# Optimization experiments

Measured on AMD Instinct MI355X. Metric: run time of the kernel, lower is better.

The kernel has to match this reference:

```python
import jax, jax.numpy as jnp
import numpy as np

N, D, DB, E, H = 1024, 512, 64, 32768, 1024

def setup_inputs() -> dict:
    key = jax.random.key(0)
    k = jax.random.split(key, 6)
    object_feats = jax.random.normal(k[0], (N, D), dtype=jnp.float32)
    bboxes_embedding = jax.random.normal(k[1], (N, N, DB), dtype=jnp.float32)
    pairs = jax.random.randint(k[2], (E, 2), 0, N, dtype=jnp.int64)
    # Kaiming-normal-ish init for the two Linear layers
    W1 = jax.random.normal(k[3], (D + D + DB, H), dtype=jnp.float32) * np.sqrt(2.0 / (D + D + DB))
    b1 = jnp.zeros((H,), dtype=jnp.float32)
    W2 = jax.random.normal(k[4], (H, D), dtype=jnp.float32) * np.sqrt(2.0 / H)
    b2 = jnp.zeros((D,), dtype=jnp.float32)
    return {"object_feats": object_feats, "bboxes_embedding": bboxes_embedding,
            "pairs": pairs, "W1": W1, "b1": b1, "W2": W2, "b2": b2}

def reference(object_feats, bboxes_embedding, pairs, W1, b1, W2, b2):
    sub = pairs[:, 0]
    obj = pairs[:, 1]
    # gather pair features: [E, D] each, plus pairwise bbox embedding [E, DB]
    f_sub = object_feats[sub]
    f_obj = object_feats[obj]
    bb = bboxes_embedding[sub, obj]
    x = jnp.concatenate((f_sub, f_obj, bb), axis=1)  # [E, 2D+DB]
    h = jax.nn.relu(x @ W1 + b1)
    out = h @ W2 + b2  # [E, D]
    n = object_feats.shape[0]
    # scatter-mean into subject nodes; each node's own feature is included once,
    # so new_feat[i] = (object_feats[i] + sum_{pairs with sub==i} out) / (1 + count[i]).
    # Nodes with no incident pairs keep their original feature (count==0 -> identity).
    seg_sum = jax.ops.segment_sum(out, sub, num_segments=n)  # [N, D]
    count = jax.ops.segment_sum(jnp.ones((out.shape[0],), dtype=out.dtype), sub, num_segments=n)
    new_feats = (object_feats + seg_sum) / (1.0 + count)[:, None]
    return (new_feats, bboxes_embedding, pairs)
```

## Files before the change

kernel.cpp:

```cpp
#include <hip/hip_runtime.h>

#define N_OBJ 1024
#define E_P   32768

typedef float f32x4 __attribute__((ext_vector_type(4)));
typedef short bf16x8 __attribute__((ext_vector_type(8)));
typedef unsigned short u16x4 __attribute__((ext_vector_type(4)));

__device__ __forceinline__ unsigned short f2bf(float f) {
    unsigned u = __float_as_uint(f);
    u = u + 0x7FFFu + ((u >> 16) & 1u);
    return (unsigned short)(u >> 16);
}

#define OFF_A    0
#define LEN_A    2097152
#define OFF_B    (OFF_A + LEN_A)
#define LEN_B    2621440
#define OFF_SEG  (OFF_B + LEN_B)
#define LEN_SEG  9437184
#define OFF_OUT  (OFF_SEG + LEN_SEG)
#define LEN_OUT  2621440

__device__ __forceinline__ void copy_role(const float4* __restrict__ src,
                                          float4* __restrict__ dst,
                                          int off, int len, int nb, int cb) {
    int stride = nb * 256;
    int i = off + cb * 256 + threadIdx.x;
    int end = off + len;
    for (; i + stride < end; i += 2 * stride) {
        float4 a = src[i];
        float4 b = src[i + stride];
        dst[i] = a;
        dst[i + stride] = b;
    }
    if (i < end) dst[i] = src[i];
}

__global__ __launch_bounds__(256) void k_a(const float* __restrict__ W1,
                                           const float* __restrict__ W2,
                                           const float* __restrict__ feats,
                                           const int* __restrict__ pairs,
                                           unsigned short* __restrict__ w1pqT,
                                           unsigned short* __restrict__ w1cT,
                                           unsigned short* __restrict__ w2T,
                                           unsigned short* __restrict__ featsb,
                                           float* __restrict__ out_pairs,
                                           int* __restrict__ counts,
                                           int* __restrict__ rank,
                                           const float4* __restrict__ csrc,
                                           float4* __restrict__ cdst) {
    int bid = blockIdx.x, tid = threadIdx.x;
    if ((bid % 3) == 2) { copy_role(csrc, cdst, OFF_A, LEN_A, 1056, bid / 3); return; }
    int job = (bid / 3) * 2 + (bid % 3);
    if (job >= 1856) {
        int i = (job - 1856) * 256 + tid;
        out_pairs[i] = (float)pairs[i];
        if (i < E_P) rank[i] = atomicAdd(&counts[pairs[2 * i]], 1);
        return;
    }
    if (job >= 1600) {
        int base = (job - 1600) * 2048 + tid * 8;
        float4 v0 = *(const float4*)&feats[base];
        float4 v1 = *(const float4*)&feats[base + 4];
        u16x4 o0 = { f2bf(v0.x), f2bf(v0.y), f2bf(v0.z), f2bf(v0.w) };
        u16x4 o1 = { f2bf(v1.x), f2bf(v1.y), f2bf(v1.z), f2bf(v1.w) };
        *(u16x4*)&featsb[base] = o0;
        *(u16x4*)&featsb[base + 4] = o1;
        return;
    }
    const float* in; unsigned short* out;
    int LDI, LDO, r0, c0, nbase, kbase;
    if (job < 1024) {
        r0 = (job >> 5) * 32; c0 = (job & 31) * 32;
        in = W1; LDI = 1024; out = w1pqT; LDO = 512;
        nbase = c0 + (r0 >= 512 ? 1024 : 0); kbase = r0 & 511;
    } else if (job < 1088) {
        int t = job - 1024; r0 = 1024 + (t >> 5) * 32; c0 = (t & 31) * 32;
        in = W1; LDI = 1024; out = w1cT; LDO = 64;
        nbase = c0; kbase = r0 - 1024;
    } else {
        int t = job - 1088; r0 = (t >> 4) * 32; c0 = (t & 15) * 32;
        in = W2; LDI = 512; out = w2T; LDO = 1024;
        nbase = c0; kbase = r0;
    }
    __shared__ float lds[32][33];
    int ti = tid >> 3, tj = (tid & 7) * 4;
    float4 v = *(const float4*)&in[(size_t)(r0 + ti) * LDI + c0 + tj];
    lds[ti][tj] = v.x; lds[ti][tj + 1] = v.y; lds[ti][tj + 2] = v.z; lds[ti][tj + 3] = v.w;
    __syncthreads();
    int oc = tid >> 3, oj = (tid & 7) * 4;
    u16x4 o = { f2bf(lds[oj][oc]), f2bf(lds[oj + 1][oc]),
                f2bf(lds[oj + 2][oc]), f2bf(lds[oj + 3][oc]) };
    *(u16x4*)&out[(size_t)(nbase + oc) * LDO + kbase + oj] = o;
}

__global__ __launch_bounds__(256) void k_b(const int* __restrict__ counts,
                                           const int* __restrict__ rank,
                                           const int* __restrict__ pairs,
                                           int* __restrict__ csr_obj,
                                           unsigned* __restrict__ brec,
                                           int* __restrict__ bcnt,
                                           const unsigned short* __restrict__ featsb,
                                           const unsigned short* __restrict__ w1pqT,
                                           const float* __restrict__ b1,
                                           float* __restrict__ P, float* __restrict__ Q,
                                           const float4* __restrict__ csrc,
                                           float4* __restrict__ cdst) {
    int bid = blockIdx.x, tid = threadIdx.x;
    if ((bid & 1) == 0) { copy_role(csrc, cdst, OFF_B, LEN_B, 672, bid >> 1); return; }
    int role = bid >> 1;
    if (role >= 641) return;

    if (role >= 129) {
        int job = role - 129;
        int m0 = (job >> 5) * 64, n0 = (job & 31) * 64;
        int w = tid >> 6, l = tid & 63;
        int ln = l & 15, kb = (l >> 4) * 8;
        int row = m0 + w * 16 + ln;
        f32x4 acc[4] = {};
        for (int k0 = 0; k0 < 512; k0 += 32) {
            bf16x8 a = *(const bf16x8*)&featsb[(size_t)row * 512 + k0 + kb];
            #pragma unroll
            for (int f = 0; f < 4; ++f) {
                bf16x8 b = *(const bf16x8*)&w1pqT[(size_t)(n0 + f * 16 + ln) * 512 + k0 + kb];
                acc[f] = __builtin_amdgcn_mfma_f32_16x16x32_bf16(a, b, acc[f], 0, 0, 0);
            }
        }
        int mr = m0 + w * 16 + (l >> 4) * 4;
        if (n0 < 1024) {
            #pragma unroll
            for (int f = 0; f < 4; ++f) {
                int n = n0 + f * 16 + ln;
                float b1v = b1[n];
                #pragma unroll
                for (int r = 0; r < 4; ++r)
                    P[(size_t)(mr + r) * 1024 + n] = acc[f][r] + b1v;
            }
        } else {
            #pragma unroll
            for (int f = 0; f < 4; ++f) {
                int n = n0 - 1024 + f * 16 + ln;
                #pragma unroll
                for (int r = 0; r < 4; ++r)
                    Q[(size_t)(mr + r) * 1024 + n] = acc[f][r];
            }
        }
        return;
    }

    __shared__ int sbuf[2][256];
    __shared__ int soff[1024];
    int c[4]; int s = 0;
    #pragma unroll
    for (int i = 0; i < 4; ++i) { c[i] = counts[tid * 4 + i]; s += c[i]; }
    sbuf[0][tid] = s;
    __syncthreads();
    int sel = 0;
    for (int d = 1; d < 256; d <<= 1) {
        int v = sbuf[sel][tid];
        if (tid >= d) v += sbuf[sel][tid - d];
        sbuf[sel ^ 1][tid] = v;
        sel ^= 1;
        __syncthreads();
    }
    int base = sbuf[sel][tid] - s;
    int run = base;
    #pragma unroll
    for (int i = 0; i < 4; ++i) { soff[tid * 4 + i] = run; run += c[i]; }
    __syncthreads();

    if (role >= 1) {
        int e = (role - 1) * 256 + tid;
        int sub = pairs[2 * e];
        csr_obj[soff[sub] + rank[e]] = pairs[2 * e + 1];
        return;
    }

    int nb[4]; int t = 0;
    #pragma unroll
    for (int i = 0; i < 4; ++i) { nb[i] = (c[i] + 31) >> 5; t += nb[i]; }
    __syncthreads();
    sbuf[0][tid] = t;
    __syncthreads();
    sel = 0;
    for (int d = 1; d < 256; d <<= 1) {
        int v = sbuf[sel][tid];
        if (tid >= d) v += sbuf[sel][tid - d];
        sbuf[sel ^ 1][tid] = v;
        sel ^= 1;
        __syncthreads();
    }
    int bpos = sbuf[sel][tid] - t;
    int run2 = base;
    #pragma unroll
    for (int i = 0; i < 4; ++i) {
        int seg = tid * 4 + i;
        for (int k = 0; k < nb[i]; ++k) {
            int st = run2 + k * 32;
            int cnt = c[i] - k * 32; if (cnt > 32) cnt = 32;
            brec[bpos++] = (unsigned)st | ((unsigned)seg << 16) | ((unsigned)(cnt - 1) << 26);
        }
        run2 += c[i];
    }
    if (tid == 255) bcnt[0] = bpos;
}

__global__ __launch_bounds__(256) void k_seg(const int* __restrict__ csr_obj,
                                             const unsigned* __restrict__ brec,
                                             const int* __restrict__ bcnt,
                                             const float* __restrict__ bb,
                                             const unsigned short* __restrict__ w1cT,
                                             const float* __restrict__ P,
                                             const float* __restrict__ Q,
                                             float* __restrict__ HS,
                                             const float4* __restrict__ csrc,
                                             float4* __restrict__ cdst) {
    int bid = blockIdx.x;
    if ((bid % 2) == 0) { copy_role(csrc, cdst, OFF_SEG, LEN_SEG, 2048, bid / 2); return; }
    int b = bid / 2;
    if (b >= bcnt[0]) return;
    unsigned rec = brec[b];
    const int start = rec & 0xFFFF;
    const int seg = (rec >> 16) & 0x3FF;
    const int n = ((rec >> 26) & 31) + 1;

    const int tid = threadIdx.x, w = tid >> 6, l = tid & 63;
    const int ln = l & 15, g4 = l >> 4, kb = g4 * 8;
    const int n0 = w * 256;
    const int nA = n < 16 ? n : 16;
    const int nB = n - 16;

    int iA = start + (ln < nA ? ln : nA - 1);
    int iB = (nB > 0) ? (start + 16 + (ln < nB ? ln : nB - 1)) : iA;
    int objA = csr_obj[iA];
    int objB = csr_obj[iB];

    const float* brA = &bb[((size_t)seg * 1024 + (size_t)objA) * 64];
    const float* brB = &bb[((size_t)seg * 1024 + (size_t)objB) * 64];
    float4 a0 = *(const float4*)&brA[kb];
    float4 a1 = *(const float4*)&brA[kb + 4];
    float4 a2 = *(const float4*)&brA[32 + kb];
    float4 a3 = *(const float4*)&brA[32 + kb + 4];
    float4 c0 = *(const float4*)&brB[kb];
    float4 c1 = *(const float4*)&brB[kb + 4];
    float4 c2 = *(const float4*)&brB[32 + kb];
    float4 c3 = *(const float4*)&brB[32 + kb + 4];
    bf16x8 A0a, A1a, A0b, A1b;
    A0a[0] = (short)f2bf(a0.x); A0a[1] = (short)f2bf(a0.y); A0a[2] = (short)f2bf(a0.z); A0a[3] = (short)f2bf(a0.w);
    A0a[4] = (short)f2bf(a1.x); A0a[5] = (short)f2bf(a1.y); A0a[6] = (short)f2bf(a1.z); A0a[7] = (short)f2bf(a1.w);
    A1a[0] = (short)f2bf(a2.x); A1a[1] = (short)f2bf(a2.y); A1a[2] = (short)f2bf(a2.z); A1a[3] = (short)f2bf(a2.w);
    A1a[4] = (short)f2bf(a3.x); A1a[5] = (short)f2bf(a3.y); A1a[6] = (short)f2bf(a3.z); A1a[7] = (short)f2bf(a3.w);
    A0b[0] = (short)f2bf(c0.x); A0b[1] = (short)f2bf(c0.y); A0b[2] = (short)f2bf(c0.z); A0b[3] = (short)f2bf(c0.w);
    A0b[4] = (short)f2bf(c1.x); A0b[5] = (short)f2bf(c1.y); A0b[6] = (short)f2bf(c1.z); A0b[7] = (short)f2bf(c1.w);
    A1b[0] = (short)f2bf(c2.x); A1b[1] = (short)f2bf(c2.y); A1b[2] = (short)f2bf(c2.z); A1b[3] = (short)f2bf(c2.w);
    A1b[4] = (short)f2bf(c3.x); A1b[5] = (short)f2bf(c3.y); A1b[6] = (short)f2bf(c3.z); A1b[7] = (short)f2bf(c3.w);

    int raA0 = __shfl(objA, g4 * 4 + 0), raA1 = __shfl(objA, g4 * 4 + 1);
    int raA2 = __shfl(objA, g4 * 4 + 2), raA3 = __shfl(objA, g4 * 4 + 3);
    int raB0 = __shfl(objB, g4 * 4 + 0), raB1 = __shfl(objB, g4 * 4 + 1);
    int raB2 = __shfl(objB, g4 * 4 + 2), raB3 = __shfl(objB, g4 * 4 + 3);
    bool vA0 = (g4 * 4 + 0) < nA, vA1 = (g4 * 4 + 1) < nA;
    bool vA2 = (g4 * 4 + 2) < nA, vA3 = (g4 * 4 + 3) < nA;
    bool vB0 = (g4 * 4 + 0) < nB, vB1 = (g4 * 4 + 1) < nB;
    bool vB2 = (g4 * 4 + 2) < nB, vB3 = (g4 * 4 + 3) < nB;

    #pragma unroll 4
    for (int f = 0; f < 16; ++f) {
        int col = n0 + f * 16 + ln;
        const unsigned short* wr = &w1cT[(size_t)col * 64];
        bf16x8 b0 = *(const bf16x8*)&wr[kb];
        bf16x8 b1 = *(const bf16x8*)&wr[32 + kb];
        f32x4 dA = {0.f, 0.f, 0.f, 0.f};
        dA = __builtin_amdgcn_mfma_f32_16x16x32_bf16(A0a, b0, dA, 0, 0, 0);
        dA = __builtin_amdgcn_mfma_f32_16x16x32_bf16(A1a, b1, dA, 0, 0, 0);
        f32x4 dB = {0.f, 0.f, 0.f, 0.f};
        dB = __builtin_amdgcn_mfma_f32_16x16x32_bf16(A0b, b0, dB, 0, 0, 0);
        dB = __builtin_amdgcn_mfma_f32_16x16x32_bf16(A1b, b1, dB, 0, 0, 0);
        float pv = P[(size_t)seg * 1024 + col];
        float qA0 = Q[(size_t)raA0 * 1024 + col];
        float qA1 = Q[(size_t)raA1 * 1024 + col];
        float qA2 = Q[(size_t)raA2 * 1024 + col];
        float qA3 = Q[(size_t)raA3 * 1024 + col];
        float qB0 = Q[(size_t)raB0 * 1024 + col];
        float qB1 = Q[(size_t)raB1 * 1024 + col];
        float qB2 = Q[(size_t)raB2 * 1024 + col];
        float qB3 = Q[(size_t)raB3 * 1024 + col];
        float h = 0.f;
        h += vA0 ? fmaxf(dA[0] + pv + qA0, 0.f) : 0.f;
        h += vA1 ? fmaxf(dA[1] + pv + qA1, 0.f) : 0.f;
        h += vA2 ? fmaxf(dA[2] + pv + qA2, 0.f) : 0.f;
        h += vA3 ? fmaxf(dA[3] + pv + qA3, 0.f) : 0.f;
        h += vB0 ? fmaxf(dB[0] + pv + qB0, 0.f) : 0.f;
        h += vB1 ? fmaxf(dB[1] + pv + qB1, 0.f) : 0.f;
        h += vB2 ? fmaxf(dB[2] + pv + qB2, 0.f) : 0.f;
        h += vB3 ? fmaxf(dB[3] + pv + qB3, 0.f) : 0.f;
        h += __shfl_xor(h, 16);
        h += __shfl_xor(h, 32);
        if (l < 16) atomicAdd(&HS[(size_t)seg * 1024 + n0 + f * 16 + l], h);
    }
}

__global__ __launch_bounds__(256) void k_out(const float* __restrict__ HS,
                                             const unsigned short* __restrict__ w2T,
                                             const float* __restrict__ feats,
                                             const float* __restrict__ b2,
                                             const int* __restrict__ counts,
                                             float* __restrict__ out0,
                                             const float4* __restrict__ csrc,
                                             float4* __restrict__ cdst) {
    int bid = blockIdx.x;
    if ((bid % 9) != 8) { copy_role(csrc, cdst, OFF_OUT, LEN_OUT, 1024, (bid / 9) * 8 + (bid % 9)); return; }
    int job = bid / 9;
    int m0 = (job >> 3) * 64, n0 = (job & 7) * 64;
    int tid = threadIdx.x, w = tid >> 6, l = tid & 63;
    int ln = l & 15, kb = (l >> 4) * 8;
    int row = m0 + w * 16 + ln;
    f32x4 acc[4] = {};
    for (int k0 = 0; k0 < 1024; k0 += 32) {
        const float* hp = &HS[(size_t)row * 1024 + k0 + kb];
        float4 h0 = *(const float4*)&hp[0];
        float4 h1 = *(const float4*)&hp[4];
        bf16x8 a;
        a[0] = (short)f2bf(h0.x); a[1] = (short)f2bf(h0.y); a[2] = (short)f2bf(h0.z); a[3] = (short)f2bf(h0.w);
        a[4] = (short)f2bf(h1.x); a[5] = (short)f2bf(h1.y); a[6] = (short)f2bf(h1.z); a[7] = (short)f2bf(h1.w);
        #pragma unroll
        for (int f = 0; f < 4; ++f) {
            bf16x8 b = *(const bf16x8*)&w2T[(size_t)(n0 + f * 16 + ln) * 1024 + k0 + kb];
            acc[f] = __builtin_amdgcn_mfma_f32_16x16x32_bf16(a, b, acc[f], 0, 0, 0);
        }
    }
    int mr = m0 + w * 16 + (l >> 4) * 4;
    float cv[4], inv[4];
    #pragma unroll
    for (int r = 0; r < 4; ++r) {
        float c = (float)counts[mr + r];
        cv[r] = c;
        inv[r] = 1.0f / (1.0f + c);
    }
    #pragma unroll
    for (int f = 0; f < 4; ++f) {
        int n = n0 + f * 16 + ln;
        float b2v = b2[n];
        #pragma unroll
        for (int r = 0; r < 4; ++r) {
            float fv = feats[(size_t)(mr + r) * 512 + n];
            out0[(size_t)(mr + r) * 512 + n] = (fv + acc[f][r] + cv[r] * b2v) * inv[r];
        }
    }
}

extern "C" void kernel_launch(void* const* d_in, const int* in_sizes, int n_in,
                              void* d_out, int out_size, void* d_ws, size_t ws_size,
                              hipStream_t stream) {
    const float* feats = (const float*)d_in[0];
    const float* bb    = (const float*)d_in[1];
    const int*   pairs = (const int*)d_in[2];
    const float* W1    = (const float*)d_in[3];
    const float* b1    = (const float*)d_in[4];
    const float* W2    = (const float*)d_in[5];
    const float* b2    = (const float*)d_in[6];

    float* out        = (float*)d_out;
    float* out_feats  = out;
    float* out_bb     = out + (size_t)N_OBJ * 512;
    float* out_pairs  = out + (size_t)N_OBJ * 512 + (size_t)N_OBJ * N_OBJ * 64;

    char* w = (char*)d_ws;
    unsigned short* featsb = (unsigned short*)w;
    unsigned short* w1pqT  = (unsigned short*)(w + (1u << 20));
    float*          HS     = (float*)w;
    unsigned short* w1cT   = (unsigned short*)(w + (4u << 20));
    unsigned short* w2T    = (unsigned short*)(w + (4u << 20) + (128u << 10));
    float* P = (float*)(w + (5u << 20) + (128u << 10));
    float* Q = (float*)(w + (9u << 20) + (128u << 10));
    char* ints = w + (13u << 20) + (128u << 10);
    int*      counts  = (int*)ints;
    int*      csr_obj = (int*)(ints + 4096);
    unsigned* brec    = (unsigned*)(ints + 4096 + 131072);
    int*      bcnt    = (int*)(ints + 4096 + 131072 + 16384);
    int*      rank    = (int*)(ints + 4096 + 131072 + 16384 + 64);

    const float4* cbb  = (const float4*)bb;
    float4*       cobb = (float4*)out_bb;

    hipMemsetAsync(counts, 0, 4096, stream);

    k_a<<<3168, 256, 0, stream>>>(W1, W2, feats, pairs, w1pqT, w1cT, w2T, featsb,
                                  out_pairs, counts, rank, cbb, cobb);
    k_b<<<1344, 256, 0, stream>>>(counts, rank, pairs, csr_obj, brec, bcnt,
                                  featsb, w1pqT, b1, P, Q, cbb, cobb);

    hipMemsetAsync(HS, 0, (size_t)N_OBJ * 1024 * sizeof(float), stream);

    k_seg<<<4096, 256, 0, stream>>>(csr_obj, brec, bcnt, bb, w1cT, P, Q, HS, cbb, cobb);
    k_out<<<1152, 256, 0, stream>>>(HS, w2T, feats, b2, counts, out_feats, cbb, cobb);
}
```

Before: 229.7 us.

## Redistribute bbox copy across kernels, drop copy from k_seg, hoist P loads

```diff
diff --git a/kernel.cpp b/kernel.cpp
--- a/kernel.cpp
+++ b/kernel.cpp
@@ -14,13 +14,11 @@
 }
 
 #define OFF_A    0
-#define LEN_A    2097152
+#define LEN_A    4194304
 #define OFF_B    (OFF_A + LEN_A)
-#define LEN_B    2621440
-#define OFF_SEG  (OFF_B + LEN_B)
-#define LEN_SEG  9437184
-#define OFF_OUT  (OFF_SEG + LEN_SEG)
-#define LEN_OUT  2621440
+#define LEN_B    5242880
+#define OFF_OUT  (OFF_B + LEN_B)
+#define LEN_OUT  7340032
 
 __device__ __forceinline__ void copy_role(const float4* __restrict__ src,
                                           float4* __restrict__ dst,
@@ -108,9 +106,8 @@
                                            const float4* __restrict__ csrc,
                                            float4* __restrict__ cdst) {
     int bid = blockIdx.x, tid = threadIdx.x;
-    if ((bid & 1) == 0) { copy_role(csrc, cdst, OFF_B, LEN_B, 672, bid >> 1); return; }
-    int role = bid >> 1;
-    if (role >= 641) return;
+    if ((bid % 3) < 2) { copy_role(csrc, cdst, OFF_B, LEN_B, 1282, (bid / 3) * 2 + (bid % 3)); return; }
+    int role = bid / 3;
 
     if (role >= 129) {
         int job = role - 129;
@@ -213,12 +210,8 @@
                                              const unsigned short* __restrict__ w1cT,
                                              const float* __restrict__ P,
                                              const float* __restrict__ Q,
-                                             float* __restrict__ HS,
-                                             const float4* __restrict__ csrc,
-                                             float4* __restrict__ cdst) {
-    int bid = blockIdx.x;
-    if ((bid % 2) == 0) { copy_role(csrc, cdst, OFF_SEG, LEN_SEG, 2048, bid / 2); return; }
-    int b = bid / 2;
+                                             float* __restrict__ HS) {
+    int b = blockIdx.x;
     if (b >= bcnt[0]) return;
     unsigned rec = brec[b];
     const int start = rec & 0xFFFF;
@@ -235,6 +228,11 @@
     int iB = (nB > 0) ? (start + 16 + (ln < nB ? ln : nB - 1)) : iA;
     int objA = csr_obj[iA];
     int objB = csr_obj[iB];
+
+    float pv[16];
+    #pragma unroll
+    for (int f = 0; f < 16; ++f)
+        pv[f] = P[(size_t)seg * 1024 + n0 + f * 16 + ln];
 
     const float* brA = &bb[((size_t)seg * 1024 + (size_t)objA) * 64];
     const float* brB = &bb[((size_t)seg * 1024 + (size_t)objB) * 64];
@@ -277,7 +275,6 @@
         f32x4 dB = {0.f, 0.f, 0.f, 0.f};
         dB = __builtin_amdgcn_mfma_f32_16x16x32_bf16(A0b, b0, dB, 0, 0, 0);
         dB = __builtin_amdgcn_mfma_f32_16x16x32_bf16(A1b, b1, dB, 0, 0, 0);
-        float pv = P[(size_t)seg * 1024 + col];
         float qA0 = Q[(size_t)raA0 * 1024 + col];
         float qA1 = Q[(size_t)raA1 * 1024 + col];
         float qA2 = Q[(size_t)raA2 * 1024 + col];
@@ -287,14 +284,14 @@
         float qB2 = Q[(size_t)raB2 * 1024 + col];
         float qB3 = Q[(size_t)raB3 * 1024 + col];
         float h = 0.f;
-        h += vA0 ? fmaxf(dA[0] + pv + qA0, 0.f) : 0.f;
-        h += vA1 ? fmaxf(dA[1] + pv + qA1, 0.f) : 0.f;
-        h += vA2 ? fmaxf(dA[2] + pv + qA2, 0.f) : 0.f;
-        h += vA3 ? fmaxf(dA[3] + pv + qA3, 0.f) : 0.f;
-        h += vB0 ? fmaxf(dB[0] + pv + qB0, 0.f) : 0.f;
-        h += vB1 ? fmaxf(dB[1] + pv + qB1, 0.f) : 0.f;
-        h += vB2 ? fmaxf(dB[2] + pv + qB2, 0.f) : 0.f;
-        h += vB3 ? fmaxf(dB[3] + pv + qB3, 0.f) : 0.f;
+        h += vA0 ? fmaxf(dA[0] + pv[f] + qA0, 0.f) : 0.f;
+        h += vA1 ? fmaxf(dA[1] + pv[f] + qA1, 0.f) : 0.f;
+        h += vA2 ? fmaxf(dA[2] + pv[f] + qA2, 0.f) : 0.f;
+        h += vA3 ? fmaxf(dA[3] + pv[f] + qA3, 0.f) : 0.f;
+        h += vB0 ? fmaxf(dB[0] + pv[f] + qB0, 0.f) : 0.f;
+        h += vB1 ? fmaxf(dB[1] + pv[f] + qB1, 0.f) : 0.f;
+        h += vB2 ? fmaxf(dB[2] + pv[f] + qB2, 0.f) : 0.f;
+        h += vB3 ? fmaxf(dB[3] + pv[f] + qB3, 0.f) : 0.f;
         h += __shfl_xor(h, 16);
         h += __shfl_xor(h, 32);
         if (l < 16) atomicAdd(&HS[(size_t)seg * 1024 + n0 + f * 16 + l], h);
@@ -310,8 +307,8 @@
                                              const float4* __restrict__ csrc,
                                              float4* __restrict__ cdst) {
     int bid = blockIdx.x;
-    if ((bid % 9) != 8) { copy_role(csrc, cdst, OFF_OUT, LEN_OUT, 1024, (bid / 9) * 8 + (bid % 9)); return; }
-    int job = bid / 9;
+    if ((bid % 17) != 16) { copy_role(csrc, cdst, OFF_OUT, LEN_OUT, 2048, (bid / 17) * 16 + (bid % 17)); return; }
+    int job = bid / 17;
     int m0 = (job >> 3) * 64, n0 = (job & 7) * 64;
     int tid = threadIdx.x, w = tid >> 6, l = tid & 63;
     int ln = l & 15, kb = (l >> 4) * 8;
@@ -388,11 +385,11 @@
 
     k_a<<<3168, 256, 0, stream>>>(W1, W2, feats, pairs, w1pqT, w1cT, w2T, featsb,
                                   out_pairs, counts, rank, cbb, cobb);
-    k_b<<<1344, 256, 0, stream>>>(counts, rank, pairs, csr_obj, brec, bcnt,
+    k_b<<<1923, 256, 0, stream>>>(counts, rank, pairs, csr_obj, brec, bcnt,
                                   featsb, w1pqT, b1, P, Q, cbb, cobb);
 
     hipMemsetAsync(HS, 0, (size_t)N_OBJ * 1024 * sizeof(float), stream);
 
-    k_seg<<<4096, 256, 0, stream>>>(csr_obj, brec, bcnt, bb, w1cT, P, Q, HS, cbb, cobb);
-    k_out<<<1152, 256, 0, stream>>>(HS, w2T, feats, b2, counts, out_feats, cbb, cobb);
-}
+    k_seg<<<2048, 256, 0, stream>>>(csr_obj, brec, bcnt, bb, w1cT, P, Q, HS);
+    k_out<<<2176, 256, 0, stream>>>(HS, w2T, feats, b2, counts, out_feats, cbb, cobb);
+}
```

After: 233.2 us. Within noise of the previous version (+1.5%).
